# Optimization experiments

Measured on AMD Instinct MI355X. Metric: run time of the kernel, lower is better.

The kernel has to match this reference:

```python
import jax, jax.numpy as jnp
import numpy as np

NEG_SLOPE = 0.2
NEG_INF = -9e15


def setup_inputs() -> dict:
    key = jax.random.key(0)
    k1, k2, k3, k4 = jax.random.split(key, 4)
    B, N, F, D = 8, 2048, 64, 64
    # dense 0/1 adjacency (float, as used in dense=True path)
    A = jax.random.randint(k1, (B, N, N), 0, 2).astype(jnp.float32)
    X = jax.random.normal(k2, (B, N, F), dtype=jnp.float32)
    # glorot on Ws [F, D]
    lim_w = float(np.sqrt(6.0 / (F + D)))
    Ws = jax.random.uniform(k3, (F, D), minval=-lim_w, maxval=lim_w, dtype=jnp.float32)
    # xavier_uniform gain=1.414 on a [2D, 1]
    lim_a = float(1.414 * np.sqrt(6.0 / (2 * D + 1)))
    a = jax.random.uniform(k4, (2 * D, 1), minval=-lim_a, maxval=lim_a, dtype=jnp.float32)
    return {"A": A, "X": X, "Ws": Ws, "a": a}


def reference(A, X, Ws, a):
    D = Ws.shape[1]
    Wh = X @ Ws                                  # [B, N, D]
    Wh1 = Wh @ a[:D, :]                          # [B, N, 1]
    Wh2 = Wh @ a[D:, :]                          # [B, N, 1]
    e = Wh1 + jnp.swapaxes(Wh2, 1, 2)            # [B, N, N]
    e = jax.nn.leaky_relu(e, negative_slope=NEG_SLOPE)
    attention = jnp.where(A > 0, A * e, NEG_INF)
    attention = jax.nn.softmax(attention, axis=2)
    H = jax.nn.elu(attention @ Wh)               # [B, N, D]
    return H
```

## Files before the change

### kernel.cpp

```cpp
#include <hip/hip_runtime.h>
#include <math.h>

typedef float f32x16 __attribute__((ext_vector_type(16)));
typedef float f32x4 __attribute__((ext_vector_type(4)));
typedef __bf16 bf16x8 __attribute__((ext_vector_type(8)));
typedef __bf16 bf16x4 __attribute__((ext_vector_type(4)));

#define N_NODES 2048
#define SCHED_FENCE() __builtin_amdgcn_sched_barrier(0)

__device__ __forceinline__ void gload16(const void* g, void* l) {
    __builtin_amdgcn_global_load_lds(
        (__attribute__((address_space(1))) void*)(uintptr_t)g,
        (__attribute__((address_space(3))) void*)l, 16, 0, 0);
}

__device__ __forceinline__ float elu1(float v) { return v > 0.f ? v : expm1f(v); }

__global__ __launch_bounds__(256) void gat_stage1(
    const float* __restrict__ X, const float* __restrict__ Ws, const float* __restrict__ av,
    __bf16* __restrict__ whT_hi, __bf16* __restrict__ whT_lo,
    float* __restrict__ sv, float* __restrict__ tvv) {
    __shared__ float xls[64][66];
    __shared__ float wss[64][64];
    __shared__ float avs[128];
    int tid = threadIdx.x;
    int b = blockIdx.x >> 5;
    int j0 = (blockIdx.x & 31) * 64;
    const float* Xb = X + ((long)(b * N_NODES + j0)) * 64;
#pragma unroll
    for (int k = 0; k < 4; ++k) {
        int i4 = k * 256 + tid;
        float4 v = *reinterpret_cast<const float4*>(Xb + i4 * 4);
        int row = i4 >> 4, c = (i4 & 15) * 4;
        *reinterpret_cast<float2*>(&xls[row][c]) = make_float2(v.x, v.y);
        *reinterpret_cast<float2*>(&xls[row][c + 2]) = make_float2(v.z, v.w);
        *reinterpret_cast<float4*>(&wss[0][0] + i4 * 4) = *reinterpret_cast<const float4*>(Ws + i4 * 4);
    }
    if (tid < 128) avs[tid] = av[tid];
    __syncthreads();
    int row = tid >> 2;
    int dblk = (tid & 3) * 16;
    float acc[16];
#pragma unroll
    for (int k = 0; k < 16; ++k) acc[k] = 0.f;
#pragma unroll 8
    for (int f = 0; f < 64; ++f) {
        float xv = xls[row][f];
        const float4* wr = reinterpret_cast<const float4*>(&wss[f][dblk]);
        float4 w0 = wr[0], w1 = wr[1], w2 = wr[2], w3 = wr[3];
        acc[0]  += xv * w0.x; acc[1]  += xv * w0.y; acc[2]  += xv * w0.z; acc[3]  += xv * w0.w;
        acc[4]  += xv * w1.x; acc[5]  += xv * w1.y; acc[6]  += xv * w1.z; acc[7]  += xv * w1.w;
        acc[8]  += xv * w2.x; acc[9]  += xv * w2.y; acc[10] += xv * w2.z; acc[11] += xv * w2.w;
        acc[12] += xv * w3.x; acc[13] += xv * w3.y; acc[14] += xv * w3.z; acc[15] += xv * w3.w;
    }
    float sp = 0.f, tp = 0.f;
#pragma unroll
    for (int k = 0; k < 16; ++k) {
        int d = dblk + k;
        __bf16 hi = (__bf16)acc[k];
        __bf16 lo = (__bf16)(acc[k] - (float)hi);
        long gidx = ((long)(b * 64 + d) << 11) + j0 + (row ^ ((d & 7) << 3));
        whT_hi[gidx] = hi;
        whT_lo[gidx] = lo;
        sp += acc[k] * avs[d];
        tp += acc[k] * avs[64 + d];
    }
    sp += __shfl_xor(sp, 1, 64); sp += __shfl_xor(sp, 2, 64);
    tp += __shfl_xor(tp, 1, 64); tp += __shfl_xor(tp, 2, 64);
    if ((tid & 3) == 0) {
        sv[b * N_NODES + j0 + row] = sp;
        tvv[b * N_NODES + j0 + row] = tp;
    }
}

__global__ __launch_bounds__(512, 4) void gat_stage2(
    const float* __restrict__ A, const __bf16* __restrict__ whT_hi, const __bf16* __restrict__ whT_lo,
    const float* __restrict__ sv, const float* __restrict__ tvv, float* __restrict__ H) {
    __shared__ __align__(16) char lds[73728];
    const int NC = 32;
    int tid = threadIdx.x;
    int nb = gridDim.x;
    int bid = ((int)blockIdx.x & 7) * (nb >> 3) + ((int)blockIdx.x >> 3);
    int b = bid >> 6;
    int it = bid & 63;
    int i0 = it * 32;
    int wid = tid >> 6, lane = tid & 63;

    int jq = tid & 15;
    int irow = tid >> 4;
    int sd = tid >> 3, sseg = tid & 7;
    const __bf16* srcHi = whT_hi + (((long)(b * 64 + sd)) << 11) + sseg * 8;
    const __bf16* srcLo = whT_lo + (((long)(b * 64 + sd)) << 11) + sseg * 8;
    int waveOff = wid * 1024;

    float s_reg = sv[b * N_NODES + i0 + irow];
    float den = 0.f;
    const float* Abase = A + ((long)(b * N_NODES + i0 + irow)) * N_NODES + jq * 4;
    const float* tb = tvv + b * N_NODES + jq * 4;

    f32x16 acc;
#pragma unroll
    for (int r = 0; r < 16; ++r) acc[r] = 0.f;

    int iAm = lane & 31;
    int dB = (wid & 1) * 32 + (lane & 31);
    int jby = (wid >> 1) * 32 + (lane >> 5) * 16;
    int offA = iAm * 128 + (jby ^ ((iAm & 7) << 4));
    int offB = dB * 128 + (jby ^ ((dB & 7) << 4));
    int wtOff = irow * 128 + ((jq * 8) ^ ((irow & 7) << 4));

    f32x4 a0, a1, a2, a3, t0, t1, t2, t3;
    { gload16(srcHi, lds + 0 * 16384 + waveOff); gload16(srcLo, lds + 0 * 16384 + waveOff + 8192); }
    { gload16(srcHi + 64, lds + 1 * 16384 + waveOff); gload16(srcLo + 64, lds + 1 * 16384 + waveOff + 8192); }
    SCHED_FENCE();
    a0 = *reinterpret_cast<const f32x4*>(Abase);
    t0 = *reinterpret_cast<const f32x4*>(tb);
    a1 = *reinterpret_cast<const f32x4*>(Abase + 64);
    t1 = *reinterpret_cast<const f32x4*>(tb + 64);
    SCHED_FENCE();

#define CHUNK_BODY(c, A_IN, T_IN, A_OUT, T_OUT)                                          \
    {                                                                                     \
        int cn = (c) + 2 < NC ? (c) + 2 : NC - 1;                                         \
        { char* dst = lds + (cn & 3) * 16384 + waveOff;                                   \
          gload16(srcHi + cn * 64, dst); gload16(srcLo + cn * 64, dst + 8192); }          \
        SCHED_FENCE();                                                                    \
        A_OUT = *reinterpret_cast<const f32x4*>(Abase + cn * 64);                         \
        T_OUT = *reinterpret_cast<const f32x4*>(tb + cn * 64);                            \
        SCHED_FENCE();                                                                    \
        { char* wt = lds + 65536 + ((c) & 1) * 4096;                                      \
          float e0 = s_reg + T_IN.x, e1 = s_reg + T_IN.y;                                 \
          float e2 = s_reg + T_IN.z, e3 = s_reg + T_IN.w;                                 \
          e0 = fmaxf(e0, 0.2f * e0); e1 = fmaxf(e1, 0.2f * e1);                           \
          e2 = fmaxf(e2, 0.2f * e2); e3 = fmaxf(e3, 0.2f * e3);                           \
          float w0 = A_IN.x * __expf(e0), w1 = A_IN.y * __expf(e1);                       \
          float w2 = A_IN.z * __expf(e2), w3 = A_IN.w * __expf(e3);                       \
          __bf16 q0 = (__bf16)w0, q1 = (__bf16)w1, q2 = (__bf16)w2, q3 = (__bf16)w3;      \
          den += (float)q0 + (float)q1 + (float)q2 + (float)q3;                           \
          bf16x4 wv = {q0, q1, q2, q3};                                                   \
          *reinterpret_cast<bf16x4*>(wt + wtOff) = wv; }                                  \
        asm volatile("s_waitcnt lgkmcnt(0)" ::: "memory");                                \
        __builtin_amdgcn_s_barrier();                                                     \
        SCHED_FENCE();                                                                    \
        { char* whb = lds + ((c) & 3) * 16384;                                            \
          char* wtb = lds + 65536 + ((c) & 1) * 4096;                                     \
          __builtin_amdgcn_s_setprio(1);                                                  \
          bf16x8 af = *reinterpret_cast<const bf16x8*>(wtb + offA);                       \
          bf16x8 bh = *reinterpret_cast<const bf16x8*>(whb + offB);                       \
          bf16x8 bl = *reinterpret_cast<const bf16x8*>(whb + 8192 + offB);                \
          acc = __builtin_amdgcn_mfma_f32_32x32x16_bf16(af, bh, acc, 0, 0, 0);            \
          acc = __builtin_amdgcn_mfma_f32_32x32x16_bf16(af, bl, acc, 0, 0, 0);            \
          __builtin_amdgcn_s_setprio(0); }                                                \
        SCHED_FENCE();                                                                    \
    }

#pragma unroll 1
    for (int c4 = 0; c4 < NC; c4 += 4) {
        CHUNK_BODY(c4 + 0, a0, t0, a2, t2)
        CHUNK_BODY(c4 + 1, a1, t1, a3, t3)
        CHUNK_BODY(c4 + 2, a2, t2, a0, t0)
        CHUNK_BODY(c4 + 3, a3, t3, a1, t1)
    }
#undef CHUNK_BODY

    asm volatile("s_waitcnt vmcnt(0)" ::: "memory");
    __syncthreads();
    {
        float* numl = (float*)(lds + (wid >> 1) * 8192);
        int colD = (wid & 1) * 32 + (lane & 31);
        int rb = 4 * (lane >> 5);
#pragma unroll
        for (int r = 0; r < 16; ++r)
            numl[((r & 3) + 8 * (r >> 2) + rb) * 64 + colD] = acc[r];
    }
#pragma unroll
    for (int off = 1; off < 16; off <<= 1) den += __shfl_xor(den, off, 64);
    float* den_lds = (float*)(lds + 65536);
    if ((tid & 15) == 0) den_lds[irow] = den;
    __syncthreads();
    {
        int row = tid >> 4, col4 = (tid & 15) * 4;
        float4 n0 = *reinterpret_cast<float4*>(lds + 0 * 8192 + row * 256 + col4 * 4);
        float4 n1 = *reinterpret_cast<float4*>(lds + 1 * 8192 + row * 256 + col4 * 4);
        float4 n2 = *reinterpret_cast<float4*>(lds + 2 * 8192 + row * 256 + col4 * 4);
        float4 n3 = *reinterpret_cast<float4*>(lds + 3 * 8192 + row * 256 + col4 * 4);
        float dinv = 1.f / den_lds[row];
        f32x4 o;
        o.x = elu1((n0.x + n1.x + n2.x + n3.x) * dinv);
        o.y = elu1((n0.y + n1.y + n2.y + n3.y) * dinv);
        o.z = elu1((n0.z + n1.z + n2.z + n3.z) * dinv);
        o.w = elu1((n0.w + n1.w + n2.w + n3.w) * dinv);
        float* Hrow = H + ((long)(b * N_NODES + i0 + row)) * 64 + col4;
        __builtin_nontemporal_store(o, reinterpret_cast<f32x4*>(Hrow));
    }
}

extern "C" void kernel_launch(void* const* d_in, const int* in_sizes, int n_in,
                              void* d_out, int out_size, void* d_ws, size_t ws_size,
                              hipStream_t stream) {
    const float* A  = (const float*)d_in[0];
    const float* X  = (const float*)d_in[1];
    const float* Ws = (const float*)d_in[2];
    const float* av = (const float*)d_in[3];
    float* H = (float*)d_out;

    char* ws = (char*)d_ws;
    __bf16* whT_hi = (__bf16*)ws;
    __bf16* whT_lo = (__bf16*)(ws + (1L << 21));
    float* sv = (float*)(ws + (1L << 22));
    float* tv = (float*)(ws + (1L << 22) + 65536);

    gat_stage1<<<256, 256, 0, stream>>>(X, Ws, av, whT_hi, whT_lo, sv, tv);
    gat_stage2<<<512, 512, 0, stream>>>(A, whT_hi, whT_lo, sv, tv, H);
}
```

Baseline: 40.44 us.

## Load Wh B-operand fragments directly into registers instead of staging through LDS

Stage 2 no longer copies the bf16 hi/lo Wh tiles into a 4-deep LDS ring with global_load_lds. Each lane instead loads its MFMA B fragments straight from global memory into registers, double-buffered one chunk ahead. Stage 1 drops its XOR swizzle to match, and the LDS footprint shrinks from 72KB to about 40KB, which could allow more blocks per CU. The cost is more vector registers and exposed global-load latency, since the prefetch distance for B falls from two chunks to one.

```diff
diff --git a/kernel.cpp b/kernel.cpp
--- a/kernel.cpp
+++ b/kernel.cpp
@@ -8,12 +8,6 @@
 
 #define N_NODES 2048
 #define SCHED_FENCE() __builtin_amdgcn_sched_barrier(0)
-
-__device__ __forceinline__ void gload16(const void* g, void* l) {
-    __builtin_amdgcn_global_load_lds(
-        (__attribute__((address_space(1))) void*)(uintptr_t)g,
-        (__attribute__((address_space(3))) void*)l, 16, 0, 0);
-}
 
 __device__ __forceinline__ float elu1(float v) { return v > 0.f ? v : expm1f(v); }
 
@@ -60,7 +54,7 @@
         int d = dblk + k;
         __bf16 hi = (__bf16)acc[k];
         __bf16 lo = (__bf16)(acc[k] - (float)hi);
-        long gidx = ((long)(b * 64 + d) << 11) + j0 + (row ^ ((d & 7) << 3));
+        long gidx = ((long)(b * 64 + d) << 11) + j0 + row;
         whT_hi[gidx] = hi;
         whT_lo[gidx] = lo;
         sp += acc[k] * avs[d];
@@ -77,7 +71,7 @@
 __global__ __launch_bounds__(512, 4) void gat_stage2(
     const float* __restrict__ A, const __bf16* __restrict__ whT_hi, const __bf16* __restrict__ whT_lo,
     const float* __restrict__ sv, const float* __restrict__ tvv, float* __restrict__ H) {
-    __shared__ __align__(16) char lds[73728];
+    __shared__ __align__(16) char lds[41216];
     const int NC = 32;
     int tid = threadIdx.x;
     int nb = gridDim.x;
@@ -89,10 +83,6 @@
 
     int jq = tid & 15;
     int irow = tid >> 4;
-    int sd = tid >> 3, sseg = tid & 7;
-    const __bf16* srcHi = whT_hi + (((long)(b * 64 + sd)) << 11) + sseg * 8;
-    const __bf16* srcLo = whT_lo + (((long)(b * 64 + sd)) << 11) + sseg * 8;
-    int waveOff = wid * 1024;
 
     float s_reg = sv[b * N_NODES + i0 + irow];
     float den = 0.f;
@@ -105,31 +95,32 @@
 
     int iAm = lane & 31;
     int dB = (wid & 1) * 32 + (lane & 31);
-    int jby = (wid >> 1) * 32 + (lane >> 5) * 16;
-    int offA = iAm * 128 + (jby ^ ((iAm & 7) << 4));
-    int offB = dB * 128 + (jby ^ ((dB & 7) << 4));
+    int colB = (wid >> 1) * 16 + (lane >> 5) * 8;
+    const __bf16* pHi = whT_hi + (((long)(b * 64 + dB)) << 11) + colB;
+    const __bf16* pLo = whT_lo + (((long)(b * 64 + dB)) << 11) + colB;
+    int offA = iAm * 128 + ((((wid >> 1) * 32) + ((lane >> 5) * 16)) ^ ((iAm & 7) << 4));
     int wtOff = irow * 128 + ((jq * 8) ^ ((irow & 7) << 4));
 
     f32x4 a0, a1, a2, a3, t0, t1, t2, t3;
-    { gload16(srcHi, lds + 0 * 16384 + waveOff); gload16(srcLo, lds + 0 * 16384 + waveOff + 8192); }
-    { gload16(srcHi + 64, lds + 1 * 16384 + waveOff); gload16(srcLo + 64, lds + 1 * 16384 + waveOff + 8192); }
-    SCHED_FENCE();
+    bf16x8 bh0, bl0, bh1, bl1;
     a0 = *reinterpret_cast<const f32x4*>(Abase);
     t0 = *reinterpret_cast<const f32x4*>(tb);
     a1 = *reinterpret_cast<const f32x4*>(Abase + 64);
     t1 = *reinterpret_cast<const f32x4*>(tb + 64);
+    bh0 = *reinterpret_cast<const bf16x8*>(pHi);
+    bl0 = *reinterpret_cast<const bf16x8*>(pLo);
     SCHED_FENCE();
 
-#define CHUNK_BODY(c, A_IN, T_IN, A_OUT, T_OUT)                                          \
+#define CHUNK_BODY(c, A_IN, T_IN, A_OUT, T_OUT, BH_CUR, BL_CUR, BH_NXT, BL_NXT)          \
     {                                                                                     \
-        int cn = (c) + 2 < NC ? (c) + 2 : NC - 1;                                         \
-        { char* dst = lds + (cn & 3) * 16384 + waveOff;                                   \
-          gload16(srcHi + cn * 64, dst); gload16(srcLo + cn * 64, dst + 8192); }          \
+        int cn2 = (c) + 2 < NC ? (c) + 2 : NC - 1;                                        \
+        int cn1 = (c) + 1 < NC ? (c) + 1 : NC - 1;                                        \
+        A_OUT = *reinterpret_cast<const f32x4*>(Abase + cn2 * 64);                        \
+        T_OUT = *reinterpret_cast<const f32x4*>(tb + cn2 * 64);                           \
+        BH_NXT = *reinterpret_cast<const bf16x8*>(pHi + cn1 * 64);                        \
+        BL_NXT = *reinterpret_cast<const bf16x8*>(pLo + cn1 * 64);                        \
         SCHED_FENCE();                                                                    \
-        A_OUT = *reinterpret_cast<const f32x4*>(Abase + cn * 64);                         \
-        T_OUT = *reinterpret_cast<const f32x4*>(tb + cn * 64);                            \
-        SCHED_FENCE();                                                                    \
-        { char* wt = lds + 65536 + ((c) & 1) * 4096;                                      \
+        { char* wt = lds + 32768 + ((c) & 1) * 4096;                                      \
           float e0 = s_reg + T_IN.x, e1 = s_reg + T_IN.y;                                 \
           float e2 = s_reg + T_IN.z, e3 = s_reg + T_IN.w;                                 \
           e0 = fmaxf(e0, 0.2f * e0); e1 = fmaxf(e1, 0.2f * e1);                           \
@@ -143,28 +134,24 @@
         asm volatile("s_waitcnt lgkmcnt(0)" ::: "memory");                                \
         __builtin_amdgcn_s_barrier();                                                     \
         SCHED_FENCE();                                                                    \
-        { char* whb = lds + ((c) & 3) * 16384;                                            \
-          char* wtb = lds + 65536 + ((c) & 1) * 4096;                                     \
+        { char* wtb = lds + 32768 + ((c) & 1) * 4096;                                     \
+          bf16x8 af = *reinterpret_cast<const bf16x8*>(wtb + offA);                       \
           __builtin_amdgcn_s_setprio(1);                                                  \
-          bf16x8 af = *reinterpret_cast<const bf16x8*>(wtb + offA);                       \
-          bf16x8 bh = *reinterpret_cast<const bf16x8*>(whb + offB);                       \
-          bf16x8 bl = *reinterpret_cast<const bf16x8*>(whb + 8192 + offB);                \
-          acc = __builtin_amdgcn_mfma_f32_32x32x16_bf16(af, bh, acc, 0, 0, 0);            \
-          acc = __builtin_amdgcn_mfma_f32_32x32x16_bf16(af, bl, acc, 0, 0, 0);            \
+          acc = __builtin_amdgcn_mfma_f32_32x32x16_bf16(af, BH_CUR, acc, 0, 0, 0);        \
+          acc = __builtin_amdgcn_mfma_f32_32x32x16_bf16(af, BL_CUR, acc, 0, 0, 0);        \
           __builtin_amdgcn_s_setprio(0); }                                                \
         SCHED_FENCE();                                                                    \
     }
 
 #pragma unroll 1
     for (int c4 = 0; c4 < NC; c4 += 4) {
-        CHUNK_BODY(c4 + 0, a0, t0, a2, t2)
-        CHUNK_BODY(c4 + 1, a1, t1, a3, t3)
-        CHUNK_BODY(c4 + 2, a2, t2, a0, t0)
-        CHUNK_BODY(c4 + 3, a3, t3, a1, t1)
+        CHUNK_BODY(c4 + 0, a0, t0, a2, t2, bh0, bl0, bh1, bl1)
+        CHUNK_BODY(c4 + 1, a1, t1, a3, t3, bh1, bl1, bh0, bl0)
+        CHUNK_BODY(c4 + 2, a2, t2, a0, t0, bh0, bl0, bh1, bl1)
+        CHUNK_BODY(c4 + 3, a3, t3, a1, t1, bh1, bl1, bh0, bl0)
     }
 #undef CHUNK_BODY
 
-    asm volatile("s_waitcnt vmcnt(0)" ::: "memory");
     __syncthreads();
     {
         float* numl = (float*)(lds + (wid >> 1) * 8192);
@@ -176,7 +163,7 @@
     }
 #pragma unroll
     for (int off = 1; off < 16; off <<= 1) den += __shfl_xor(den, off, 64);
-    float* den_lds = (float*)(lds + 65536);
+    float* den_lds = (float*)(lds + 40960);
     if ((tid & 15) == 0) den_lds[irow] = den;
     __syncthreads();
     {
```

After: 54.29 us. +34.3%, slower.

## Switch Wh to single fp16 with max-shifted exponent and halve MFMA work

Applied to the files above, without the earlier changes.

Replaces the bf16 hi/lo split of Wh with one fp16 copy, which halves the B-operand LDS traffic and global reads and removes the second MFMA per chunk. To keep fp16 attention weights in range, stage1 computes a per-batch max of t via an order-preserving atomicMax, and stage2 subtracts a per-row shift derived from it before exponentiating. LDS shrinks from 72KB to 40KB, which allows launch bounds of 6 blocks per SM, and the prefetch schedule changes to load t one chunk ahead. The risks are fp16 precision loss and a possible underflow of small weights, plus an extra memset launch and atomics.

```diff
diff --git a/kernel.cpp b/kernel.cpp
--- a/kernel.cpp
+++ b/kernel.cpp
@@ -3,8 +3,8 @@
 
 typedef float f32x16 __attribute__((ext_vector_type(16)));
 typedef float f32x4 __attribute__((ext_vector_type(4)));
-typedef __bf16 bf16x8 __attribute__((ext_vector_type(8)));
-typedef __bf16 bf16x4 __attribute__((ext_vector_type(4)));
+typedef _Float16 f16x8 __attribute__((ext_vector_type(8)));
+typedef _Float16 f16x4 __attribute__((ext_vector_type(4)));
 
 #define N_NODES 2048
 #define SCHED_FENCE() __builtin_amdgcn_sched_barrier(0)
@@ -17,10 +17,19 @@
 
 __device__ __forceinline__ float elu1(float v) { return v > 0.f ? v : expm1f(v); }
 
+__device__ __forceinline__ unsigned enc_f(float x) {
+    unsigned b = __float_as_uint(x);
+    return (b & 0x80000000u) ? ~b : (b | 0x80000000u);
+}
+__device__ __forceinline__ float dec_f(unsigned u) {
+    unsigned b = (u & 0x80000000u) ? (u ^ 0x80000000u) : ~u;
+    return __uint_as_float(b);
+}
+
 __global__ __launch_bounds__(256) void gat_stage1(
     const float* __restrict__ X, const float* __restrict__ Ws, const float* __restrict__ av,
-    __bf16* __restrict__ whT_hi, __bf16* __restrict__ whT_lo,
-    float* __restrict__ sv, float* __restrict__ tvv) {
+    _Float16* __restrict__ whT, float* __restrict__ sv, float* __restrict__ tvv,
+    unsigned* __restrict__ tmaxU) {
     __shared__ float xls[64][66];
     __shared__ float wss[64][64];
     __shared__ float avs[128];
@@ -58,11 +67,8 @@
 #pragma unroll
     for (int k = 0; k < 16; ++k) {
         int d = dblk + k;
-        __bf16 hi = (__bf16)acc[k];
-        __bf16 lo = (__bf16)(acc[k] - (float)hi);
         long gidx = ((long)(b * 64 + d) << 11) + j0 + (row ^ ((d & 7) << 3));
-        whT_hi[gidx] = hi;
-        whT_lo[gidx] = lo;
+        whT[gidx] = (_Float16)acc[k];
         sp += acc[k] * avs[d];
         tp += acc[k] * avs[64 + d];
     }
@@ -72,12 +78,17 @@
         sv[b * N_NODES + j0 + row] = sp;
         tvv[b * N_NODES + j0 + row] = tp;
     }
-}
-
-__global__ __launch_bounds__(512, 4) void gat_stage2(
-    const float* __restrict__ A, const __bf16* __restrict__ whT_hi, const __bf16* __restrict__ whT_lo,
-    const float* __restrict__ sv, const float* __restrict__ tvv, float* __restrict__ H) {
-    __shared__ __align__(16) char lds[73728];
+    float tw = tp;
+#pragma unroll
+    for (int off = 4; off < 64; off <<= 1) tw = fmaxf(tw, __shfl_xor(tw, off, 64));
+    if ((tid & 63) == 0) atomicMax(tmaxU + b, enc_f(tw));
+}
+
+__global__ __launch_bounds__(512, 6) void gat_stage2(
+    const float* __restrict__ A, const _Float16* __restrict__ whT,
+    const float* __restrict__ sv, const float* __restrict__ tvv,
+    const unsigned* __restrict__ tmaxU, float* __restrict__ H) {
+    __shared__ __align__(16) char lds[40960];
     const int NC = 32;
     int tid = threadIdx.x;
     int nb = gridDim.x;
@@ -90,11 +101,13 @@
     int jq = tid & 15;
     int irow = tid >> 4;
     int sd = tid >> 3, sseg = tid & 7;
-    const __bf16* srcHi = whT_hi + (((long)(b * 64 + sd)) << 11) + sseg * 8;
-    const __bf16* srcLo = whT_lo + (((long)(b * 64 + sd)) << 11) + sseg * 8;
+    const _Float16* src = whT + (((long)(b * 64 + sd)) << 11) + sseg * 8;
     int waveOff = wid * 1024;
 
     float s_reg = sv[b * N_NODES + i0 + irow];
+    float Tb = dec_f(tmaxU[b]);
+    float m0 = s_reg + Tb;
+    float Ci = fmaxf(m0, 0.2f * m0) - 5.0f;
     float den = 0.f;
     const float* Abase = A + ((long)(b * N_NODES + i0 + irow)) * N_NODES + jq * 4;
     const float* tb = tvv + b * N_NODES + jq * 4;
@@ -110,57 +123,55 @@
     int offB = dB * 128 + (jby ^ ((dB & 7) << 4));
     int wtOff = irow * 128 + ((jq * 8) ^ ((irow & 7) << 4));
 
-    f32x4 a0, a1, a2, a3, t0, t1, t2, t3;
-    { gload16(srcHi, lds + 0 * 16384 + waveOff); gload16(srcLo, lds + 0 * 16384 + waveOff + 8192); }
-    { gload16(srcHi + 64, lds + 1 * 16384 + waveOff); gload16(srcLo + 64, lds + 1 * 16384 + waveOff + 8192); }
+    f32x4 a0, a1, a2, a3, t0, t1;
+    a0 = *reinterpret_cast<const f32x4*>(Abase);
+    a1 = *reinterpret_cast<const f32x4*>(Abase + 64);
+    t0 = *reinterpret_cast<const f32x4*>(tb);
     SCHED_FENCE();
-    a0 = *reinterpret_cast<const f32x4*>(Abase);
-    t0 = *reinterpret_cast<const f32x4*>(tb);
-    a1 = *reinterpret_cast<const f32x4*>(Abase + 64);
-    t1 = *reinterpret_cast<const f32x4*>(tb + 64);
+    gload16(src, lds + waveOff);
+    gload16(src + 64, lds + 8192 + waveOff);
     SCHED_FENCE();
 
-#define CHUNK_BODY(c, A_IN, T_IN, A_OUT, T_OUT)                                          \
+#define CHUNK_BODY(c, A_IN, A_OUT, T_IN, T_OUT)                                          \
     {                                                                                     \
-        int cn = (c) + 2 < NC ? (c) + 2 : NC - 1;                                         \
-        { char* dst = lds + (cn & 3) * 16384 + waveOff;                                   \
-          gload16(srcHi + cn * 64, dst); gload16(srcLo + cn * 64, dst + 8192); }          \
-        SCHED_FENCE();                                                                    \
-        A_OUT = *reinterpret_cast<const f32x4*>(Abase + cn * 64);                         \
-        T_OUT = *reinterpret_cast<const f32x4*>(tb + cn * 64);                            \
-        SCHED_FENCE();                                                                    \
-        { char* wt = lds + 65536 + ((c) & 1) * 4096;                                      \
+        int cn2 = (c) + 2 < NC ? (c) + 2 : NC - 1;                                        \
+        int cn1 = (c) + 1 < NC ? (c) + 1 : NC - 1;                                        \
+        A_OUT = *reinterpret_cast<const f32x4*>(Abase + cn2 * 64);                        \
+        T_OUT = *reinterpret_cast<const f32x4*>(tb + cn1 * 64);                           \
+        SCHED_FENCE();                                                                    \
+        gload16(src + cn2 * 64, lds + (cn2 & 3) * 8192 + waveOff);                        \
+        SCHED_FENCE();                                                                    \
+        { char* wt = lds + 32768 + ((c) & 1) * 4096;                                      \
           float e0 = s_reg + T_IN.x, e1 = s_reg + T_IN.y;                                 \
           float e2 = s_reg + T_IN.z, e3 = s_reg + T_IN.w;                                 \
           e0 = fmaxf(e0, 0.2f * e0); e1 = fmaxf(e1, 0.2f * e1);                           \
           e2 = fmaxf(e2, 0.2f * e2); e3 = fmaxf(e3, 0.2f * e3);                           \
-          float w0 = A_IN.x * __expf(e0), w1 = A_IN.y * __expf(e1);                       \
-          float w2 = A_IN.z * __expf(e2), w3 = A_IN.w * __expf(e3);                       \
-          __bf16 q0 = (__bf16)w0, q1 = (__bf16)w1, q2 = (__bf16)w2, q3 = (__bf16)w3;      \
+          float w0 = A_IN.x * __expf(e0 - Ci), w1 = A_IN.y * __expf(e1 - Ci);             \
+          float w2 = A_IN.z * __expf(e2 - Ci), w3 = A_IN.w * __expf(e3 - Ci);             \
+          _Float16 q0 = (_Float16)w0, q1 = (_Float16)w1;                                  \
+          _Float16 q2 = (_Float16)w2, q3 = (_Float16)w3;                                  \
           den += (float)q0 + (float)q1 + (float)q2 + (float)q3;                           \
-          bf16x4 wv = {q0, q1, q2, q3};                                                   \
-          *reinterpret_cast<bf16x4*>(wt + wtOff) = wv; }                                  \
+          f16x4 wv = {q0, q1, q2, q3};                                                    \
+          *reinterpret_cast<f16x4*>(wt + wtOff) = wv; }                                   \
         asm volatile("s_waitcnt lgkmcnt(0)" ::: "memory");                                \
         __builtin_amdgcn_s_barrier();                                                     \
         SCHED_FENCE();                                                                    \
-        { char* whb = lds + ((c) & 3) * 16384;                                            \
-          char* wtb = lds + 65536 + ((c) & 1) * 4096;                                     \
+        { char* whb = lds + ((c) & 3) * 8192;                                             \
+          char* wtb = lds + 32768 + ((c) & 1) * 4096;                                     \
+          f16x8 af = *reinterpret_cast<const f16x8*>(wtb + offA);                         \
+          f16x8 bh = *reinterpret_cast<const f16x8*>(whb + offB);                         \
           __builtin_amdgcn_s_setprio(1);                                                  \
-          bf16x8 af = *reinterpret_cast<const bf16x8*>(wtb + offA);                       \
-          bf16x8 bh = *reinterpret_cast<const bf16x8*>(whb + offB);                       \
-          bf16x8 bl = *reinterpret_cast<const bf16x8*>(whb + 8192 + offB);                \
-          acc = __builtin_amdgcn_mfma_f32_32x32x16_bf16(af, bh, acc, 0, 0, 0);            \
-          acc = __builtin_amdgcn_mfma_f32_32x32x16_bf16(af, bl, acc, 0, 0, 0);            \
+          acc = __builtin_amdgcn_mfma_f32_32x32x16_f16(af, bh, acc, 0, 0, 0);             \
           __builtin_amdgcn_s_setprio(0); }                                                \
         SCHED_FENCE();                                                                    \
     }
 
 #pragma unroll 1
     for (int c4 = 0; c4 < NC; c4 += 4) {
-        CHUNK_BODY(c4 + 0, a0, t0, a2, t2)
-        CHUNK_BODY(c4 + 1, a1, t1, a3, t3)
-        CHUNK_BODY(c4 + 2, a2, t2, a0, t0)
-        CHUNK_BODY(c4 + 3, a3, t3, a1, t1)
+        CHUNK_BODY(c4 + 0, a0, a2, t0, t1)
+        CHUNK_BODY(c4 + 1, a1, a3, t1, t0)
+        CHUNK_BODY(c4 + 2, a2, a0, t0, t1)
+        CHUNK_BODY(c4 + 3, a3, a1, t1, t0)
     }
 #undef CHUNK_BODY
 
@@ -176,7 +187,7 @@
     }
 #pragma unroll
     for (int off = 1; off < 16; off <<= 1) den += __shfl_xor(den, off, 64);
-    float* den_lds = (float*)(lds + 65536);
+    float* den_lds = (float*)(lds + 32768);
     if ((tid & 15) == 0) den_lds[irow] = den;
     __syncthreads();
     {
@@ -206,11 +217,12 @@
     float* H = (float*)d_out;
 
     char* ws = (char*)d_ws;
-    __bf16* whT_hi = (__bf16*)ws;
-    __bf16* whT_lo = (__bf16*)(ws + (1L << 21));
-    float* sv = (float*)(ws + (1L << 22));
-    float* tv = (float*)(ws + (1L << 22) + 65536);
-
-    gat_stage1<<<256, 256, 0, stream>>>(X, Ws, av, whT_hi, whT_lo, sv, tv);
-    gat_stage2<<<512, 512, 0, stream>>>(A, whT_hi, whT_lo, sv, tv, H);
-}
+    _Float16* whT = (_Float16*)ws;
+    float* sv = (float*)(ws + (1L << 21));
+    float* tv = (float*)(ws + (1L << 21) + 65536);
+    unsigned* tmaxU = (unsigned*)(ws + (1L << 21) + 131072);
+
+    hipMemsetAsync(tmaxU, 0, 8 * sizeof(unsigned), stream);
+    gat_stage1<<<256, 256, 0, stream>>>(X, Ws, av, whT, sv, tv, tmaxU);
+    gat_stage2<<<512, 512, 0, stream>>>(A, whT, sv, tv, tmaxU, H);
+}
```

Result: slower. 52.69 us (+30.3%).

## Precompute adjacency bitmask in LDS via ballots before the attention loop

Applied to the files above, without the earlier changes.

Before the main loop, each block reads its 32 rows of the adjacency matrix with coalesced full-row loads. It packs them into 64-bit ballot masks stored in LDS. The main loop then tests mask bits to decide whether to keep exp(e), instead of streaming float adjacency values per chunk. This takes the large A stream out of the pipelined loop and shortens the loop body. The trade-off is that the A fetch becomes a serialized prologue with limited memory parallelism. LDS use grows and setprio now brackets only the MFMAs.

```diff
diff --git a/kernel.cpp b/kernel.cpp
--- a/kernel.cpp
+++ b/kernel.cpp
@@ -5,6 +5,7 @@
 typedef float f32x4 __attribute__((ext_vector_type(4)));
 typedef __bf16 bf16x8 __attribute__((ext_vector_type(8)));
 typedef __bf16 bf16x4 __attribute__((ext_vector_type(4)));
+typedef unsigned long ulong2v __attribute__((ext_vector_type(2)));
 
 #define N_NODES 2048
 #define SCHED_FENCE() __builtin_amdgcn_sched_barrier(0)
@@ -77,7 +78,7 @@
 __global__ __launch_bounds__(512, 4) void gat_stage2(
     const float* __restrict__ A, const __bf16* __restrict__ whT_hi, const __bf16* __restrict__ whT_lo,
     const float* __restrict__ sv, const float* __restrict__ tvv, float* __restrict__ H) {
-    __shared__ __align__(16) char lds[73728];
+    __shared__ __align__(16) char lds[81920];
     const int NC = 32;
     int tid = threadIdx.x;
     int nb = gridDim.x;
@@ -94,9 +95,30 @@
     const __bf16* srcLo = whT_lo + (((long)(b * 64 + sd)) << 11) + sseg * 8;
     int waveOff = wid * 1024;
 
+    unsigned long* lmask = (unsigned long*)(lds + 65536);
+
+    {
+        const float* Arow0 = A + ((long)(b * N_NODES + i0 + wid * 4)) * N_NODES;
+#pragma unroll
+        for (int rr = 0; rr < 4; ++rr) {
+            const float* Ar = Arow0 + (long)rr * N_NODES;
+#pragma unroll 2
+            for (int i = 0; i < 8; ++i) {
+                f32x4 v = *reinterpret_cast<const f32x4*>(Ar + i * 256 + lane * 4);
+                unsigned long b0 = __ballot(v.x > 0.f);
+                unsigned long b1 = __ballot(v.y > 0.f);
+                unsigned long b2 = __ballot(v.z > 0.f);
+                unsigned long b3 = __ballot(v.w > 0.f);
+                if (lane == 0) {
+                    unsigned long* mrow = &lmask[(wid * 4 + rr) * 32 + i * 4];
+                    mrow[0] = b0; mrow[1] = b1; mrow[2] = b2; mrow[3] = b3;
+                }
+            }
+        }
+    }
+
     float s_reg = sv[b * N_NODES + i0 + irow];
     float den = 0.f;
-    const float* Abase = A + ((long)(b * N_NODES + i0 + irow)) * N_NODES + jq * 4;
     const float* tb = tvv + b * N_NODES + jq * 4;
 
     f32x16 acc;
@@ -110,32 +132,34 @@
     int offB = dB * 128 + (jby ^ ((dB & 7) << 4));
     int wtOff = irow * 128 + ((jq * 8) ^ ((irow & 7) << 4));
 
-    f32x4 a0, a1, a2, a3, t0, t1, t2, t3;
-    { gload16(srcHi, lds + 0 * 16384 + waveOff); gload16(srcLo, lds + 0 * 16384 + waveOff + 8192); }
-    { gload16(srcHi + 64, lds + 1 * 16384 + waveOff); gload16(srcLo + 64, lds + 1 * 16384 + waveOff + 8192); }
+    __syncthreads();
+
+    f32x4 t0, t1, t2, t3;
+    { char* dst = lds + waveOff; gload16(srcHi, dst); gload16(srcLo, dst + 8192); }
+    { char* dst = lds + 16384 + waveOff; gload16(srcHi + 64, dst); gload16(srcLo + 64, dst + 8192); }
     SCHED_FENCE();
-    a0 = *reinterpret_cast<const f32x4*>(Abase);
     t0 = *reinterpret_cast<const f32x4*>(tb);
-    a1 = *reinterpret_cast<const f32x4*>(Abase + 64);
     t1 = *reinterpret_cast<const f32x4*>(tb + 64);
     SCHED_FENCE();
 
-#define CHUNK_BODY(c, A_IN, T_IN, A_OUT, T_OUT)                                          \
+#define CHUNK_BODY(c, K, T_IN, T_OUT, M0, M1, M2, M3)                                    \
     {                                                                                     \
         int cn = (c) + 2 < NC ? (c) + 2 : NC - 1;                                         \
         { char* dst = lds + (cn & 3) * 16384 + waveOff;                                   \
           gload16(srcHi + cn * 64, dst); gload16(srcLo + cn * 64, dst + 8192); }          \
         SCHED_FENCE();                                                                    \
-        A_OUT = *reinterpret_cast<const f32x4*>(Abase + cn * 64);                         \
         T_OUT = *reinterpret_cast<const f32x4*>(tb + cn * 64);                            \
         SCHED_FENCE();                                                                    \
-        { char* wt = lds + 65536 + ((c) & 1) * 4096;                                      \
+        { char* wt = lds + 73728 + ((c) & 1) * 4096;                                      \
+          int l_ = (K) * 16 + jq;                                                         \
           float e0 = s_reg + T_IN.x, e1 = s_reg + T_IN.y;                                 \
           float e2 = s_reg + T_IN.z, e3 = s_reg + T_IN.w;                                 \
           e0 = fmaxf(e0, 0.2f * e0); e1 = fmaxf(e1, 0.2f * e1);                           \
           e2 = fmaxf(e2, 0.2f * e2); e3 = fmaxf(e3, 0.2f * e3);                           \
-          float w0 = A_IN.x * __expf(e0), w1 = A_IN.y * __expf(e1);                       \
-          float w2 = A_IN.z * __expf(e2), w3 = A_IN.w * __expf(e3);                       \
+          float w0 = ((M0 >> l_) & 1UL) ? __expf(e0) : 0.f;                               \
+          float w1 = ((M1 >> l_) & 1UL) ? __expf(e1) : 0.f;                               \
+          float w2 = ((M2 >> l_) & 1UL) ? __expf(e2) : 0.f;                               \
+          float w3 = ((M3 >> l_) & 1UL) ? __expf(e3) : 0.f;                               \
           __bf16 q0 = (__bf16)w0, q1 = (__bf16)w1, q2 = (__bf16)w2, q3 = (__bf16)w3;      \
           den += (float)q0 + (float)q1 + (float)q2 + (float)q3;                           \
           bf16x4 wv = {q0, q1, q2, q3};                                                   \
@@ -144,11 +168,11 @@
         __builtin_amdgcn_s_barrier();                                                     \
         SCHED_FENCE();                                                                    \
         { char* whb = lds + ((c) & 3) * 16384;                                            \
-          char* wtb = lds + 65536 + ((c) & 1) * 4096;                                     \
-          __builtin_amdgcn_s_setprio(1);                                                  \
+          char* wtb = lds + 73728 + ((c) & 1) * 4096;                                     \
           bf16x8 af = *reinterpret_cast<const bf16x8*>(wtb + offA);                       \
           bf16x8 bh = *reinterpret_cast<const bf16x8*>(whb + offB);                       \
           bf16x8 bl = *reinterpret_cast<const bf16x8*>(whb + 8192 + offB);                \
+          __builtin_amdgcn_s_setprio(1);                                                  \
           acc = __builtin_amdgcn_mfma_f32_32x32x16_bf16(af, bh, acc, 0, 0, 0);            \
           acc = __builtin_amdgcn_mfma_f32_32x32x16_bf16(af, bl, acc, 0, 0, 0);            \
           __builtin_amdgcn_s_setprio(0); }                                                \
@@ -157,10 +181,13 @@
 
 #pragma unroll 1
     for (int c4 = 0; c4 < NC; c4 += 4) {
-        CHUNK_BODY(c4 + 0, a0, t0, a2, t2)
-        CHUNK_BODY(c4 + 1, a1, t1, a3, t3)
-        CHUNK_BODY(c4 + 2, a2, t2, a0, t0)
-        CHUNK_BODY(c4 + 3, a3, t3, a1, t1)
+        ulong2v mA = *reinterpret_cast<const ulong2v*>(&lmask[irow * 32 + c4]);
+        ulong2v mB = *reinterpret_cast<const ulong2v*>(&lmask[irow * 32 + c4 + 2]);
+        unsigned long m0 = mA.x, m1 = mA.y, m2 = mB.x, m3 = mB.y;
+        CHUNK_BODY(c4 + 0, 0, t0, t2, m0, m1, m2, m3)
+        CHUNK_BODY(c4 + 1, 1, t1, t3, m0, m1, m2, m3)
+        CHUNK_BODY(c4 + 2, 2, t2, t0, m0, m1, m2, m3)
+        CHUNK_BODY(c4 + 3, 3, t3, t1, m0, m1, m2, m3)
     }
 #undef CHUNK_BODY
 
@@ -176,7 +203,7 @@
     }
 #pragma unroll
     for (int off = 1; off < 16; off <<= 1) den += __shfl_xor(den, off, 64);
-    float* den_lds = (float*)(lds + 65536);
+    float* den_lds = (float*)(lds + 73728);
     if ((tid & 15) == 0) den_lds[irow] = den;
     __syncthreads();
     {
```

After: 55.58 us. 37.4% more time.
